# Optimization experiments

Measured on AMD Instinct MI355X. Metric: run time of the kernel, lower is better.

## Reference

```python
import jax, jax.numpy as jnp
import numpy as np

N_NODES = 50000
N_EDGES = 600000
N_GRAPHS = 64
IN_C, HID_C, OUT_C = 128, 128, 64


def gcn_conv(x, edge_index, W, b, num_nodes):
    """PyG GCNConv: x' = D^-1/2 (A + I) D^-1/2 (x W) + b, messages src->dst."""
    src, dst = edge_index[0], edge_index[1]
    # add self-loops
    loop = jnp.arange(num_nodes, dtype=src.dtype)
    src_full = jnp.concatenate([src, loop])
    dst_full = jnp.concatenate([dst, loop])
    # degree of A+I counted at the aggregation (dst) side
    deg = jax.ops.segment_sum(jnp.ones_like(dst_full, dtype=x.dtype), dst_full,
                              num_segments=num_nodes)
    dinv = jax.lax.rsqrt(jnp.maximum(deg, 1.0))
    norm = dinv[src_full] * dinv[dst_full]              # [E+N]
    h = x @ W                                           # [N, C_out] dense GEMM
    msg = h[src_full] * norm[:, None]                   # gather + scale
    out = jax.ops.segment_sum(msg, dst_full, num_segments=num_nodes)  # scatter-add
    return out + b


def global_mean_pool(x, batch, num_graphs):
    s = jax.ops.segment_sum(x, batch, num_segments=num_graphs)
    cnt = jax.ops.segment_sum(jnp.ones_like(batch, dtype=x.dtype), batch,
                              num_segments=num_graphs)
    return s / jnp.maximum(cnt, 1.0)[:, None]


def setup_inputs() -> dict:
    key = jax.random.key(0)
    ks = jax.random.split(key, 8)
    x = jax.random.normal(ks[0], (N_NODES, IN_C), dtype=jnp.float32)
    edge_index = jax.random.randint(ks[1], (2, N_EDGES), 0, N_NODES, dtype=jnp.int64)
    batch = jnp.sort(jax.random.randint(ks[2], (N_NODES,), 0, N_GRAPHS, dtype=jnp.int64))
    # Glorot-style init like PyG defaults
    W1 = jax.random.normal(ks[3], (IN_C, HID_C), dtype=jnp.float32) * (1.0 / np.sqrt(IN_C))
    b1 = jnp.zeros((HID_C,), dtype=jnp.float32)
    W2 = jax.random.normal(ks[4], (HID_C, OUT_C), dtype=jnp.float32) * (1.0 / np.sqrt(HID_C))
    b2 = jnp.zeros((OUT_C,), dtype=jnp.float32)
    return {"x": x, "W1": W1, "b1": b1, "W2": W2, "b2": b2,
            "edge_index": edge_index, "batch": batch}


def reference(x, W1, b1, W2, b2, edge_index, batch):
    h = gcn_conv(x, edge_index, W1, b1, N_NODES)
    h = jax.nn.relu(h)
    h = gcn_conv(h, edge_index, W2, b2, N_NODES)
    return global_mean_pool(h, batch, N_GRAPHS)  # [N_GRAPHS, OUT_C]
```

## Files before the change

kernel.cpp:

```cpp
#include <hip/hip_runtime.h>

#define NN 50000
#define NE 600000
#define NG 64
#define SCAN_T 1024
#define SCAN_NB ((NN + SCAN_T - 1) / SCAN_T)
#define PSPLIT 16

typedef unsigned int uint_t;
typedef unsigned short ushort_t;
typedef __attribute__((ext_vector_type(8))) short bf16x8;
typedef __attribute__((ext_vector_type(4))) float f32x4;

__device__ __forceinline__ ushort_t f2bf(float x) {
    uint_t u = __builtin_bit_cast(uint_t, x);
    u = (u + 0x7FFFu + ((u >> 16) & 1u)) >> 16;
    return (ushort_t)u;
}
__device__ __forceinline__ float bf_lo(uint_t p) {
    uint_t v = p << 16; return __builtin_bit_cast(float, v);
}
__device__ __forceinline__ float bf_hi(uint_t p) {
    uint_t v = p & 0xFFFF0000u; return __builtin_bit_cast(float, v);
}

__global__ void k_zero_deg(int* __restrict__ deg) {
    int i = blockIdx.x * blockDim.x + threadIdx.x;
    if (i < NN) deg[i] = 0;
}

__global__ void k_hist(const int* __restrict__ dst, int* __restrict__ deg) {
    int e = blockIdx.x * blockDim.x + threadIdx.x;
    if (e < NE) atomicAdd(&deg[dst[e]], 1);
}

__global__ void k_wprep(const float* __restrict__ W1, const float* __restrict__ W2,
                        ushort_t* __restrict__ W1t, ushort_t* __restrict__ W2t) {
    int idx = blockIdx.x * 256 + threadIdx.x;
    if (idx < 128 * 128) {
        int k = idx >> 7, n = idx & 127;
        W1t[n * 128 + k] = f2bf(W1[idx]);
    } else if (idx < 128 * 128 + 128 * 64) {
        int j = idx - 128 * 128;
        int k = j >> 6, n = j & 63;
        W2t[n * 128 + k] = f2bf(W2[j]);
    }
}

__global__ __launch_bounds__(SCAN_T) void k_scan1(const int* __restrict__ deg,
                                                  int* __restrict__ blockSums) {
    __shared__ int s[SCAN_T];
    int i = blockIdx.x * SCAN_T + threadIdx.x;
    s[threadIdx.x] = (i < NN) ? deg[i] : 0;
    __syncthreads();
    for (int off = SCAN_T / 2; off > 0; off >>= 1) {
        if (threadIdx.x < off) s[threadIdx.x] += s[threadIdx.x + off];
        __syncthreads();
    }
    if (threadIdx.x == 0) blockSums[blockIdx.x] = s[0];
}

__global__ __launch_bounds__(SCAN_T) void k_scan3(const int* __restrict__ deg,
                                                  const int* __restrict__ blockSums,
                                                  int* __restrict__ rowptr,
                                                  int* __restrict__ cursor,
                                                  float* __restrict__ dinv) {
    __shared__ int offs[64];
    __shared__ int s[SCAN_T];
    const int t = threadIdx.x;
    if (t < 64) {
        int orig = (t < SCAN_NB) ? blockSums[t] : 0;
        int v = orig;
        for (int off = 1; off < 64; off <<= 1) {
            int u = __shfl_up(v, off);
            if (t >= off) v += u;
        }
        offs[t] = v - orig;
    }
    const int i = blockIdx.x * SCAN_T + t;
    const int v = (i < NN) ? deg[i] : 0;
    s[t] = v;
    __syncthreads();
    for (int off = 1; off < SCAN_T; off <<= 1) {
        int u = (t >= off) ? s[t - off] : 0;
        int cur = s[t];
        __syncthreads();
        s[t] = cur + u;
        __syncthreads();
    }
    if (i < NN) {
        int ex = offs[blockIdx.x] + s[t] - v;
        rowptr[i] = ex;
        cursor[i] = ex;
        dinv[i] = rsqrtf((float)(v + 1));
    }
    if (i == 0) rowptr[NN] = NE;
}

__global__ void k_scatter(const int* __restrict__ src, const int* __restrict__ dst,
                          int* __restrict__ cursor, int* __restrict__ csr_src) {
    int e = blockIdx.x * blockDim.x + threadIdx.x;
    if (e >= NE) return;
    int d = dst[e];
    int p = atomicAdd(&cursor[d], 1);
    csr_src[p] = src[e];
}

__global__ __launch_bounds__(256) void k_gemm_mfma(const float* __restrict__ X,
                                                   const ushort_t* __restrict__ Wt,
                                                   const float* __restrict__ dinv,
                                                   ushort_t* __restrict__ Hb) {
    __shared__ ushort_t xs[128 * 128];
    __shared__ ushort_t ws[128 * 128];
    const int tid = threadIdx.x;
    const int row0 = blockIdx.x * 128;

    for (int idx = tid; idx < 128 * 32; idx += 256) {
        int r = idx >> 5, c4 = idx & 31;
        int row = row0 + r;
        float4 v = make_float4(0.f, 0.f, 0.f, 0.f);
        if (row < NN) v = ((const float4*)X)[(long)row * 32 + c4];
        ushort4 o;
        o.x = f2bf(v.x); o.y = f2bf(v.y); o.z = f2bf(v.z); o.w = f2bf(v.w);
        uint_t byte = (uint_t)(r * 256 + c4 * 8) ^ (uint_t)((r & 7) << 4);
        *(ushort4*)((char*)xs + byte) = o;
    }
    for (int idx = tid; idx < 128 * 16; idx += 256) {
        int n = idx >> 4, c16 = idx & 15;
        uint4 v = ((const uint4*)Wt)[idx];
        uint_t byte = (uint_t)(n * 256 + c16 * 16) ^ (uint_t)((n & 7) << 4);
        *(uint4*)((char*)ws + byte) = v;
    }
    __syncthreads();

    const int w = tid >> 6;
    const int l = tid & 63;
    const int m0 = (w >> 1) * 4;
    const int n0 = (w & 1) * 4;
    const int lr = l & 15;
    const int kg = l >> 4;

    f32x4 acc[4][4] = {};
    for (int kk = 0; kk < 4; ++kk) {
        const int kb = kk * 64 + kg * 16;
        bf16x8 a[4], b[4];
#pragma unroll
        for (int m = 0; m < 4; ++m) {
            int r = (m0 + m) * 16 + lr;
            uint_t byte = (uint_t)(r * 256 + kb) ^ (uint_t)((r & 7) << 4);
            a[m] = *(const bf16x8*)((const char*)xs + byte);
        }
#pragma unroll
        for (int n = 0; n < 4; ++n) {
            int r = (n0 + n) * 16 + lr;
            uint_t byte = (uint_t)(r * 256 + kb) ^ (uint_t)((r & 7) << 4);
            b[n] = *(const bf16x8*)((const char*)ws + byte);
        }
#pragma unroll
        for (int m = 0; m < 4; ++m)
#pragma unroll
            for (int n = 0; n < 4; ++n)
                acc[m][n] = __builtin_amdgcn_mfma_f32_16x16x32_bf16(a[m], b[n], acc[m][n], 0, 0, 0);
    }

#pragma unroll
    for (int m = 0; m < 4; ++m) {
#pragma unroll
        for (int r = 0; r < 4; ++r) {
            int row = row0 + (m0 + m) * 16 + kg * 4 + r;
            if (row < NN) {
                float sc = dinv[row];
#pragma unroll
                for (int n = 0; n < 4; ++n) {
                    int col = (n0 + n) * 16 + lr;
                    Hb[(long)row * 128 + col] = f2bf(acc[m][n][r] * sc);
                }
            }
        }
    }
}

__global__ __launch_bounds__(256) void k_gemm_mfma2(const ushort_t* __restrict__ H1,
                                                    const ushort_t* __restrict__ W2t,
                                                    const float* __restrict__ dinv,
                                                    ushort_t* __restrict__ G) {
    __shared__ ushort_t xs[128 * 128];
    __shared__ ushort_t ws2[64 * 128];
    const int tid = threadIdx.x;
    const int row0 = blockIdx.x * 128;

    for (int idx = tid; idx < 128 * 16; idx += 256) {
        int r = idx >> 4, c16 = idx & 15;
        int row = row0 + r;
        uint4 v = make_uint4(0u, 0u, 0u, 0u);
        if (row < NN) v = ((const uint4*)H1)[(long)row * 16 + c16];
        uint_t byte = (uint_t)(r * 256 + c16 * 16) ^ (uint_t)((r & 7) << 4);
        *(uint4*)((char*)xs + byte) = v;
    }
    for (int idx = tid; idx < 64 * 16; idx += 256) {
        int n = idx >> 4, c16 = idx & 15;
        uint4 v = ((const uint4*)W2t)[idx];
        uint_t byte = (uint_t)(n * 256 + c16 * 16) ^ (uint_t)((n & 7) << 4);
        *(uint4*)((char*)ws2 + byte) = v;
    }
    __syncthreads();

    const int w = tid >> 6;
    const int l = tid & 63;
    const int lr = l & 15;
    const int kg = l >> 4;
    const int m0 = w * 2;

    f32x4 acc[2][4] = {};
    for (int kk = 0; kk < 4; ++kk) {
        const int kb = kk * 64 + kg * 16;
        bf16x8 a[2], b[4];
#pragma unroll
        for (int m = 0; m < 2; ++m) {
            int r = (m0 + m) * 16 + lr;
            uint_t byte = (uint_t)(r * 256 + kb) ^ (uint_t)((r & 7) << 4);
            a[m] = *(const bf16x8*)((const char*)xs + byte);
        }
#pragma unroll
        for (int n = 0; n < 4; ++n) {
            int r = n * 16 + lr;
            uint_t byte = (uint_t)(r * 256 + kb) ^ (uint_t)((r & 7) << 4);
            b[n] = *(const bf16x8*)((const char*)ws2 + byte);
        }
#pragma unroll
        for (int m = 0; m < 2; ++m)
#pragma unroll
            for (int n = 0; n < 4; ++n)
                acc[m][n] = __builtin_amdgcn_mfma_f32_16x16x32_bf16(a[m], b[n], acc[m][n], 0, 0, 0);
    }

#pragma unroll
    for (int m = 0; m < 2; ++m) {
#pragma unroll
        for (int r = 0; r < 4; ++r) {
            int row = row0 + (m0 + m) * 16 + kg * 4 + r;
            if (row < NN) {
                float sc = dinv[row];
#pragma unroll
                for (int n = 0; n < 4; ++n) {
                    int col = n * 16 + lr;
                    G[(long)row * 64 + col] = f2bf(acc[m][n][r] * sc);
                }
            }
        }
    }
}

template <int C, int EPI>
__global__ __launch_bounds__(256) void k_agg(const int* __restrict__ rowptr,
                                             const int* __restrict__ csr_src,
                                             const float* __restrict__ dinv,
                                             const ushort_t* __restrict__ Hb,
                                             const float* __restrict__ bias,
                                             ushort_t* __restrict__ OUT) {
    constexpr int TPN = C / 8;
    constexpr int NPB = 256 / TPN;
    const int node = blockIdx.x * NPB + threadIdx.x / TPN;
    if (node >= NN) return;
    const int lane = threadIdx.x % TPN;
    const float dd = dinv[node];
    const uint4* __restrict__ H4 = (const uint4*)Hb;

    float a0, a1, a2, a3, a4, a5, a6, a7;
    {
        uint4 sv = H4[(long)node * TPN + lane];
        a0 = bf_lo(sv.x); a1 = bf_hi(sv.x);
        a2 = bf_lo(sv.y); a3 = bf_hi(sv.y);
        a4 = bf_lo(sv.z); a5 = bf_hi(sv.z);
        a6 = bf_lo(sv.w); a7 = bf_hi(sv.w);
    }

    const int beg = rowptr[node], end = rowptr[node + 1];
    int k = beg;
    const int n4 = beg + ((end - beg) & ~3);
    for (; k < n4; k += 4) {
        int s0 = csr_src[k + 0];
        int s1 = csr_src[k + 1];
        int s2 = csr_src[k + 2];
        int s3 = csr_src[k + 3];
        uint4 h0 = H4[(long)s0 * TPN + lane];
        uint4 h1 = H4[(long)s1 * TPN + lane];
        uint4 h2 = H4[(long)s2 * TPN + lane];
        uint4 h3 = H4[(long)s3 * TPN + lane];
        a0 += (bf_lo(h0.x) + bf_lo(h1.x)) + (bf_lo(h2.x) + bf_lo(h3.x));
        a1 += (bf_hi(h0.x) + bf_hi(h1.x)) + (bf_hi(h2.x) + bf_hi(h3.x));
        a2 += (bf_lo(h0.y) + bf_lo(h1.y)) + (bf_lo(h2.y) + bf_lo(h3.y));
        a3 += (bf_hi(h0.y) + bf_hi(h1.y)) + (bf_hi(h2.y) + bf_hi(h3.y));
        a4 += (bf_lo(h0.z) + bf_lo(h1.z)) + (bf_lo(h2.z) + bf_lo(h3.z));
        a5 += (bf_hi(h0.z) + bf_hi(h1.z)) + (bf_hi(h2.z) + bf_hi(h3.z));
        a6 += (bf_lo(h0.w) + bf_lo(h1.w)) + (bf_lo(h2.w) + bf_lo(h3.w));
        a7 += (bf_hi(h0.w) + bf_hi(h1.w)) + (bf_hi(h2.w) + bf_hi(h3.w));
    }
    for (; k < end; ++k) {
        int s = csr_src[k];
        uint4 h = H4[(long)s * TPN + lane];
        a0 += bf_lo(h.x); a1 += bf_hi(h.x);
        a2 += bf_lo(h.y); a3 += bf_hi(h.y);
        a4 += bf_lo(h.z); a5 += bf_hi(h.z);
        a6 += bf_lo(h.w); a7 += bf_hi(h.w);
    }

    a0 *= dd; a1 *= dd; a2 *= dd; a3 *= dd;
    a4 *= dd; a5 *= dd; a6 *= dd; a7 *= dd;

    if (EPI == 0) {
        const float4 b0 = *(const float4*)&bias[lane * 8];
        const float4 b1 = *(const float4*)&bias[lane * 8 + 4];
        a0 = fmaxf(a0 + b0.x, 0.f); a1 = fmaxf(a1 + b0.y, 0.f);
        a2 = fmaxf(a2 + b0.z, 0.f); a3 = fmaxf(a3 + b0.w, 0.f);
        a4 = fmaxf(a4 + b1.x, 0.f); a5 = fmaxf(a5 + b1.y, 0.f);
        a6 = fmaxf(a6 + b1.z, 0.f); a7 = fmaxf(a7 + b1.w, 0.f);
    }
    uint4 o;
    o.x = (uint_t)f2bf(a0) | ((uint_t)f2bf(a1) << 16);
    o.y = (uint_t)f2bf(a2) | ((uint_t)f2bf(a3) << 16);
    o.z = (uint_t)f2bf(a4) | ((uint_t)f2bf(a5) << 16);
    o.w = (uint_t)f2bf(a6) | ((uint_t)f2bf(a7) << 16);
    ((uint4*)OUT)[(long)node * TPN + lane] = o;
}

__global__ __launch_bounds__(256) void k_pool1(const ushort_t* __restrict__ V,
                                               const int* __restrict__ batch,
                                               float* __restrict__ partial) {
    const int g = blockIdx.x / PSPLIT;
    const int s = blockIdx.x % PSPLIT;
    int beg, end;
    {
        int lo = 0, hi = NN;
        while (lo < hi) { int mid = (lo + hi) >> 1; if (batch[mid] < g) lo = mid + 1; else hi = mid; }
        beg = lo;
        lo = beg; hi = NN;
        while (lo < hi) { int mid = (lo + hi) >> 1; if (batch[mid] < g + 1) lo = mid + 1; else hi = mid; }
        end = lo;
    }
    const int c = threadIdx.x & 15;
    const int rg = threadIdx.x >> 4;
    const uint2* __restrict__ V2 = (const uint2*)V;

    float4 acc = make_float4(0.f, 0.f, 0.f, 0.f);
    for (int n = beg + s * 16 + rg; n < end; n += PSPLIT * 16) {
        uint2 h = V2[(long)n * 16 + c];
        acc.x += bf_lo(h.x); acc.y += bf_hi(h.x);
        acc.z += bf_lo(h.y); acc.w += bf_hi(h.y);
    }
    __shared__ float4 red[16][17];
    red[rg][c] = acc;
    __syncthreads();
    if (rg == 0) {
        float4 t = red[0][c];
#pragma unroll
        for (int i = 1; i < 16; ++i) {
            float4 u = red[i][c];
            t.x += u.x; t.y += u.y; t.z += u.z; t.w += u.w;
        }
        ((float4*)partial)[(long)blockIdx.x * 16 + c] = t;
    }
}

__global__ __launch_bounds__(64) void k_pool2(const float* __restrict__ partial,
                                              const int* __restrict__ batch,
                                              const float* __restrict__ b2,
                                              float* __restrict__ out) {
    const int g = blockIdx.x;
    const int ch = threadIdx.x;
    int beg, end;
    {
        int lo = 0, hi = NN;
        while (lo < hi) { int mid = (lo + hi) >> 1; if (batch[mid] < g) lo = mid + 1; else hi = mid; }
        beg = lo;
        lo = beg; hi = NN;
        while (lo < hi) { int mid = (lo + hi) >> 1; if (batch[mid] < g + 1) lo = mid + 1; else hi = mid; }
        end = lo;
    }
    float s = 0.f;
    for (int i = 0; i < PSPLIT; ++i) s += partial[(long)(g * PSPLIT + i) * 64 + ch];
    int cnt = end - beg;
    out[g * 64 + ch] = (cnt > 0) ? (s / (float)cnt + b2[ch]) : 0.f;
}

extern "C" void kernel_launch(void* const* d_in, const int* in_sizes, int n_in,
                              void* d_out, int out_size, void* d_ws, size_t ws_size,
                              hipStream_t stream) {
    const float* x  = (const float*)d_in[0];
    const float* W1 = (const float*)d_in[1];
    const float* b1 = (const float*)d_in[2];
    const float* W2 = (const float*)d_in[3];
    const float* b2 = (const float*)d_in[4];
    const int* ei   = (const int*)d_in[5];
    const int* src  = ei;
    const int* dst  = ei + NE;
    const int* batch = (const int*)d_in[6];
    float* out = (float*)d_out;

    char* p = (char*)d_ws;
    int* deg       = (int*)p;          p += (size_t)NN * 4;
    int* rowptr    = (int*)p;          p += (size_t)(NN + 4) * 4;
    int* cursor    = (int*)p;          p += (size_t)NN * 4;
    int* csr_src   = (int*)p;          p += (size_t)NE * 4;
    int* blockSums = (int*)p;          p += (size_t)64 * 4;
    float* dinv    = (float*)p;        p += (size_t)NN * 4;
    float* partial = (float*)p;        p += (size_t)NG * PSPLIT * 64 * 4;
    ushort_t* W1t  = (ushort_t*)p;     p += (size_t)128 * 128 * 2;
    ushort_t* W2t  = (ushort_t*)p;     p += (size_t)64 * 128 * 2;
    ushort_t* Hb   = (ushort_t*)p;     p += (size_t)NN * 128 * 2;
    ushort_t* H1b  = (ushort_t*)p;     p += (size_t)NN * 128 * 2;
    ushort_t* Gb   = (ushort_t*)p;     p += (size_t)NN * 64 * 2;
    ushort_t* Vb   = (ushort_t*)p;     p += (size_t)NN * 64 * 2;

    k_wprep<<<96, 256, 0, stream>>>(W1, W2, W1t, W2t);
    k_zero_deg<<<(NN + 255) / 256, 256, 0, stream>>>(deg);
    k_hist<<<(NE + 255) / 256, 256, 0, stream>>>(dst, deg);
    k_scan1<<<SCAN_NB, SCAN_T, 0, stream>>>(deg, blockSums);
    k_scan3<<<SCAN_NB, SCAN_T, 0, stream>>>(deg, blockSums, rowptr, cursor, dinv);
    k_scatter<<<(NE + 255) / 256, 256, 0, stream>>>(src, dst, cursor, csr_src);

    k_gemm_mfma<<<(NN + 127) / 128, 256, 0, stream>>>(x, W1t, dinv, Hb);
    k_agg<128, 0><<<(NN + 15) / 16, 256, 0, stream>>>(rowptr, csr_src, dinv, Hb, b1, H1b);

    k_gemm_mfma2<<<(NN + 127) / 128, 256, 0, stream>>>(H1b, W2t, dinv, Gb);
    k_agg<64, 1><<<(NN + 31) / 32, 256, 0, stream>>>(rowptr, csr_src, dinv, Gb, b1 , Vb);

    k_pool1<<<NG * PSPLIT, 256, 0, stream>>>(Vb, batch, partial);
    k_pool2<<<NG, 64, 0, stream>>>(partial, batch, b2, out);
}
```

Baseline: 159.1 us.

## Fuse CSR build into cooperative kernel and fuse layer-2 aggregation with pooling

```diff
diff --git a/kernel.cpp b/kernel.cpp
--- a/kernel.cpp
+++ b/kernel.cpp
@@ -1,11 +1,14 @@
 #include <hip/hip_runtime.h>
+#include <hip/hip_cooperative_groups.h>
+
+namespace cg = cooperative_groups;
 
 #define NN 50000
 #define NE 600000
 #define NG 64
 #define SCAN_T 1024
 #define SCAN_NB ((NN + SCAN_T - 1) / SCAN_T)
-#define PSPLIT 16
+#define COOP_NB 256
 
 typedef unsigned int uint_t;
 typedef unsigned short ushort_t;
@@ -24,86 +27,85 @@
     uint_t v = p & 0xFFFF0000u; return __builtin_bit_cast(float, v);
 }
 
-__global__ void k_zero_deg(int* __restrict__ deg) {
-    int i = blockIdx.x * blockDim.x + threadIdx.x;
-    if (i < NN) deg[i] = 0;
-}
-
-__global__ void k_hist(const int* __restrict__ dst, int* __restrict__ deg) {
-    int e = blockIdx.x * blockDim.x + threadIdx.x;
-    if (e < NE) atomicAdd(&deg[dst[e]], 1);
-}
-
-__global__ void k_wprep(const float* __restrict__ W1, const float* __restrict__ W2,
-                        ushort_t* __restrict__ W1t, ushort_t* __restrict__ W2t) {
-    int idx = blockIdx.x * 256 + threadIdx.x;
-    if (idx < 128 * 128) {
-        int k = idx >> 7, n = idx & 127;
-        W1t[n * 128 + k] = f2bf(W1[idx]);
-    } else if (idx < 128 * 128 + 128 * 64) {
-        int j = idx - 128 * 128;
-        int k = j >> 6, n = j & 63;
-        W2t[n * 128 + k] = f2bf(W2[j]);
-    }
-}
-
-__global__ __launch_bounds__(SCAN_T) void k_scan1(const int* __restrict__ deg,
-                                                  int* __restrict__ blockSums) {
-    __shared__ int s[SCAN_T];
-    int i = blockIdx.x * SCAN_T + threadIdx.x;
-    s[threadIdx.x] = (i < NN) ? deg[i] : 0;
-    __syncthreads();
-    for (int off = SCAN_T / 2; off > 0; off >>= 1) {
-        if (threadIdx.x < off) s[threadIdx.x] += s[threadIdx.x + off];
-        __syncthreads();
-    }
-    if (threadIdx.x == 0) blockSums[blockIdx.x] = s[0];
-}
-
-__global__ __launch_bounds__(SCAN_T) void k_scan3(const int* __restrict__ deg,
-                                                  const int* __restrict__ blockSums,
+__global__ __launch_bounds__(SCAN_T) void k_build(const float* __restrict__ W1,
+                                                  const float* __restrict__ W2,
+                                                  const int* __restrict__ src,
+                                                  const int* __restrict__ dst,
+                                                  ushort_t* __restrict__ W1t,
+                                                  ushort_t* __restrict__ W2t,
+                                                  int* __restrict__ deg,
+                                                  int* __restrict__ blockSums,
                                                   int* __restrict__ rowptr,
                                                   int* __restrict__ cursor,
-                                                  float* __restrict__ dinv) {
-    __shared__ int offs[64];
+                                                  float* __restrict__ dinv,
+                                                  float* __restrict__ psum,
+                                                  int* __restrict__ csr_src) {
+    cg::grid_group grid = cg::this_grid();
+    const int tid = threadIdx.x;
+    const int gtid = blockIdx.x * SCAN_T + tid;
+    const int GT = COOP_NB * SCAN_T;
+
+    for (int i = gtid; i < NN; i += GT) deg[i] = 0;
+    for (int i = gtid; i < NG * 64; i += GT) psum[i] = 0.f;
+    for (int i = gtid; i < 128 * 128; i += GT) {
+        int k = i >> 7, n = i & 127;
+        W1t[n * 128 + k] = f2bf(W1[i]);
+    }
+    for (int i = gtid; i < 128 * 64; i += GT) {
+        int k = i >> 6, n = i & 63;
+        W2t[n * 128 + k] = f2bf(W2[i]);
+    }
+    grid.sync();
+
+    for (int e = gtid; e < NE; e += GT) atomicAdd(&deg[dst[e]], 1);
+    grid.sync();
+
     __shared__ int s[SCAN_T];
-    const int t = threadIdx.x;
-    if (t < 64) {
-        int orig = (t < SCAN_NB) ? blockSums[t] : 0;
-        int v = orig;
-        for (int off = 1; off < 64; off <<= 1) {
-            int u = __shfl_up(v, off);
-            if (t >= off) v += u;
-        }
-        offs[t] = v - orig;
-    }
-    const int i = blockIdx.x * SCAN_T + t;
-    const int v = (i < NN) ? deg[i] : 0;
-    s[t] = v;
-    __syncthreads();
-    for (int off = 1; off < SCAN_T; off <<= 1) {
-        int u = (t >= off) ? s[t - off] : 0;
-        int cur = s[t];
+    __shared__ int offs_s;
+    int v = 0;
+    if (blockIdx.x < SCAN_NB) {
+        int i = blockIdx.x * SCAN_T + tid;
+        v = (i < NN) ? deg[i] : 0;
+        s[tid] = v;
         __syncthreads();
-        s[t] = cur + u;
+        for (int off = 1; off < SCAN_T; off <<= 1) {
+            int u = (tid >= off) ? s[tid - off] : 0;
+            int cur = s[tid];
+            __syncthreads();
+            s[tid] = cur + u;
+            __syncthreads();
+        }
+        if (tid == SCAN_T - 1) blockSums[blockIdx.x] = s[SCAN_T - 1];
+    }
+    grid.sync();
+
+    if (blockIdx.x < SCAN_NB) {
+        if (tid < 64) {
+            int orig = (tid < SCAN_NB) ? blockSums[tid] : 0;
+            int w = orig;
+            for (int off = 1; off < 64; off <<= 1) {
+                int u = __shfl_up(w, off);
+                if (tid >= off) w += u;
+            }
+            if (tid == (int)blockIdx.x) offs_s = w - orig;
+        }
         __syncthreads();
-    }
-    if (i < NN) {
-        int ex = offs[blockIdx.x] + s[t] - v;
-        rowptr[i] = ex;
-        cursor[i] = ex;
-        dinv[i] = rsqrtf((float)(v + 1));
-    }
-    if (i == 0) rowptr[NN] = NE;
-}
-
-__global__ void k_scatter(const int* __restrict__ src, const int* __restrict__ dst,
-                          int* __restrict__ cursor, int* __restrict__ csr_src) {
-    int e = blockIdx.x * blockDim.x + threadIdx.x;
-    if (e >= NE) return;
-    int d = dst[e];
-    int p = atomicAdd(&cursor[d], 1);
-    csr_src[p] = src[e];
+        int i = blockIdx.x * SCAN_T + tid;
+        if (i < NN) {
+            int ex = offs_s + s[tid] - v;
+            rowptr[i] = ex;
+            cursor[i] = ex;
+            dinv[i] = rsqrtf((float)(v + 1));
+        }
+        if (i == 0) rowptr[NN] = NE;
+    }
+    grid.sync();
+
+    for (int e = gtid; e < NE; e += GT) {
+        int d = dst[e];
+        int p = atomicAdd(&cursor[d], 1);
+        csr_src[p] = src[e];
+    }
 }
 
 __global__ __launch_bounds__(256) void k_gemm_mfma(const float* __restrict__ X,
@@ -251,14 +253,13 @@
     }
 }
 
-template <int C, int EPI>
-__global__ __launch_bounds__(256) void k_agg(const int* __restrict__ rowptr,
-                                             const int* __restrict__ csr_src,
-                                             const float* __restrict__ dinv,
-                                             const ushort_t* __restrict__ Hb,
-                                             const float* __restrict__ bias,
-                                             ushort_t* __restrict__ OUT) {
-    constexpr int TPN = C / 8;
+__global__ __launch_bounds__(256) void k_agg1(const int* __restrict__ rowptr,
+                                              const int* __restrict__ csr_src,
+                                              const float* __restrict__ dinv,
+                                              const ushort_t* __restrict__ Hb,
+                                              const float* __restrict__ bias,
+                                              ushort_t* __restrict__ OUT) {
+    constexpr int TPN = 16;
     constexpr int NPB = 256 / TPN;
     const int node = blockIdx.x * NPB + threadIdx.x / TPN;
     if (node >= NN) return;
@@ -308,14 +309,13 @@
     a0 *= dd; a1 *= dd; a2 *= dd; a3 *= dd;
     a4 *= dd; a5 *= dd; a6 *= dd; a7 *= dd;
 
-    if (EPI == 0) {
-        const float4 b0 = *(const float4*)&bias[lane * 8];
-        const float4 b1 = *(const float4*)&bias[lane * 8 + 4];
-        a0 = fmaxf(a0 + b0.x, 0.f); a1 = fmaxf(a1 + b0.y, 0.f);
-        a2 = fmaxf(a2 + b0.z, 0.f); a3 = fmaxf(a3 + b0.w, 0.f);
-        a4 = fmaxf(a4 + b1.x, 0.f); a5 = fmaxf(a5 + b1.y, 0.f);
-        a6 = fmaxf(a6 + b1.z, 0.f); a7 = fmaxf(a7 + b1.w, 0.f);
-    }
+    const float4 b0 = *(const float4*)&bias[lane * 8];
+    const float4 b1 = *(const float4*)&bias[lane * 8 + 4];
+    a0 = fmaxf(a0 + b0.x, 0.f); a1 = fmaxf(a1 + b0.y, 0.f);
+    a2 = fmaxf(a2 + b0.z, 0.f); a3 = fmaxf(a3 + b0.w, 0.f);
+    a4 = fmaxf(a4 + b1.x, 0.f); a5 = fmaxf(a5 + b1.y, 0.f);
+    a6 = fmaxf(a6 + b1.z, 0.f); a7 = fmaxf(a7 + b1.w, 0.f);
+
     uint4 o;
     o.x = (uint_t)f2bf(a0) | ((uint_t)f2bf(a1) << 16);
     o.y = (uint_t)f2bf(a2) | ((uint_t)f2bf(a3) << 16);
@@ -324,45 +324,88 @@
     ((uint4*)OUT)[(long)node * TPN + lane] = o;
 }
 
-__global__ __launch_bounds__(256) void k_pool1(const ushort_t* __restrict__ V,
-                                               const int* __restrict__ batch,
-                                               float* __restrict__ partial) {
-    const int g = blockIdx.x / PSPLIT;
-    const int s = blockIdx.x % PSPLIT;
-    int beg, end;
-    {
-        int lo = 0, hi = NN;
-        while (lo < hi) { int mid = (lo + hi) >> 1; if (batch[mid] < g) lo = mid + 1; else hi = mid; }
-        beg = lo;
-        lo = beg; hi = NN;
-        while (lo < hi) { int mid = (lo + hi) >> 1; if (batch[mid] < g + 1) lo = mid + 1; else hi = mid; }
-        end = lo;
-    }
-    const int c = threadIdx.x & 15;
-    const int rg = threadIdx.x >> 4;
-    const uint2* __restrict__ V2 = (const uint2*)V;
-
-    float4 acc = make_float4(0.f, 0.f, 0.f, 0.f);
-    for (int n = beg + s * 16 + rg; n < end; n += PSPLIT * 16) {
-        uint2 h = V2[(long)n * 16 + c];
-        acc.x += bf_lo(h.x); acc.y += bf_hi(h.x);
-        acc.z += bf_lo(h.y); acc.w += bf_hi(h.y);
-    }
-    __shared__ float4 red[16][17];
-    red[rg][c] = acc;
+__global__ __launch_bounds__(256) void k_agg2pool(const int* __restrict__ rowptr,
+                                                  const int* __restrict__ csr_src,
+                                                  const float* __restrict__ dinv,
+                                                  const ushort_t* __restrict__ Gb,
+                                                  const int* __restrict__ batch,
+                                                  float* __restrict__ psum) {
+    constexpr int TPN = 8;
+    constexpr int NPB = 32;
+    const int nodeLocal = threadIdx.x / TPN;
+    const int node = blockIdx.x * NPB + nodeLocal;
+    const int lane = threadIdx.x % TPN;
+    __shared__ float vsh[NPB][64 + 1];
+    __shared__ int gsh[NPB];
+
+    if (node < NN) {
+        const float dd = dinv[node];
+        const uint4* __restrict__ H4 = (const uint4*)Gb;
+
+        float a0, a1, a2, a3, a4, a5, a6, a7;
+        {
+            uint4 sv = H4[(long)node * TPN + lane];
+            a0 = bf_lo(sv.x); a1 = bf_hi(sv.x);
+            a2 = bf_lo(sv.y); a3 = bf_hi(sv.y);
+            a4 = bf_lo(sv.z); a5 = bf_hi(sv.z);
+            a6 = bf_lo(sv.w); a7 = bf_hi(sv.w);
+        }
+        const int beg = rowptr[node], end = rowptr[node + 1];
+        int k = beg;
+        const int n4 = beg + ((end - beg) & ~3);
+        for (; k < n4; k += 4) {
+            int s0 = csr_src[k + 0];
+            int s1 = csr_src[k + 1];
+            int s2 = csr_src[k + 2];
+            int s3 = csr_src[k + 3];
+            uint4 h0 = H4[(long)s0 * TPN + lane];
+            uint4 h1 = H4[(long)s1 * TPN + lane];
+            uint4 h2 = H4[(long)s2 * TPN + lane];
+            uint4 h3 = H4[(long)s3 * TPN + lane];
+            a0 += (bf_lo(h0.x) + bf_lo(h1.x)) + (bf_lo(h2.x) + bf_lo(h3.x));
+            a1 += (bf_hi(h0.x) + bf_hi(h1.x)) + (bf_hi(h2.x) + bf_hi(h3.x));
+            a2 += (bf_lo(h0.y) + bf_lo(h1.y)) + (bf_lo(h2.y) + bf_lo(h3.y));
+            a3 += (bf_hi(h0.y) + bf_hi(h1.y)) + (bf_hi(h2.y) + bf_hi(h3.y));
+            a4 += (bf_lo(h0.z) + bf_lo(h1.z)) + (bf_lo(h2.z) + bf_lo(h3.z));
+            a5 += (bf_hi(h0.z) + bf_hi(h1.z)) + (bf_hi(h2.z) + bf_hi(h3.z));
+            a6 += (bf_lo(h0.w) + bf_lo(h1.w)) + (bf_lo(h2.w) + bf_lo(h3.w));
+            a7 += (bf_hi(h0.w) + bf_hi(h1.w)) + (bf_hi(h2.w) + bf_hi(h3.w));
+        }
+        for (; k < end; ++k) {
+            int s = csr_src[k];
+            uint4 h = H4[(long)s * TPN + lane];
+            a0 += bf_lo(h.x); a1 += bf_hi(h.x);
+            a2 += bf_lo(h.y); a3 += bf_hi(h.y);
+            a4 += bf_lo(h.z); a5 += bf_hi(h.z);
+            a6 += bf_lo(h.w); a7 += bf_hi(h.w);
+        }
+        float* vp = &vsh[nodeLocal][lane * 8];
+        vp[0] = a0 * dd; vp[1] = a1 * dd; vp[2] = a2 * dd; vp[3] = a3 * dd;
+        vp[4] = a4 * dd; vp[5] = a5 * dd; vp[6] = a6 * dd; vp[7] = a7 * dd;
+        if (lane == 0) gsh[nodeLocal] = batch[node];
+    } else {
+        if (lane == 0) gsh[nodeLocal] = -1;
+    }
     __syncthreads();
-    if (rg == 0) {
-        float4 t = red[0][c];
-#pragma unroll
-        for (int i = 1; i < 16; ++i) {
-            float4 u = red[i][c];
-            t.x += u.x; t.y += u.y; t.z += u.z; t.w += u.w;
-        }
-        ((float4*)partial)[(long)blockIdx.x * 16 + c] = t;
-    }
-}
-
-__global__ __launch_bounds__(64) void k_pool2(const float* __restrict__ partial,
+
+    if (threadIdx.x < 64) {
+        const int ch = threadIdx.x;
+        float acc = 0.f;
+        int gprev = -1;
+        for (int n = 0; n < NPB; ++n) {
+            int g = gsh[n];
+            if (g != gprev) {
+                if (gprev >= 0) unsafeAtomicAdd(&psum[gprev * 64 + ch], acc);
+                acc = 0.f;
+                gprev = g;
+            }
+            if (g >= 0) acc += vsh[n][ch];
+        }
+        if (gprev >= 0) unsafeAtomicAdd(&psum[gprev * 64 + ch], acc);
+    }
+}
+
+__global__ __launch_bounds__(64) void k_pool2(const float* __restrict__ psum,
                                               const int* __restrict__ batch,
                                               const float* __restrict__ b2,
                                               float* __restrict__ out) {
@@ -377,10 +420,8 @@
         while (lo < hi) { int mid = (lo + hi) >> 1; if (batch[mid] < g + 1) lo = mid + 1; else hi = mid; }
         end = lo;
     }
-    float s = 0.f;
-    for (int i = 0; i < PSPLIT; ++i) s += partial[(long)(g * PSPLIT + i) * 64 + ch];
     int cnt = end - beg;
-    out[g * 64 + ch] = (cnt > 0) ? (s / (float)cnt + b2[ch]) : 0.f;
+    out[g * 64 + ch] = (cnt > 0) ? (psum[g * 64 + ch] / (float)cnt + b2[ch]) : 0.f;
 }
 
 extern "C" void kernel_launch(void* const* d_in, const int* in_sizes, int n_in,
@@ -392,8 +433,8 @@
     const float* W2 = (const float*)d_in[3];
     const float* b2 = (const float*)d_in[4];
     const int* ei   = (const int*)d_in[5];
-    const int* src  = ei;
-    const int* dst  = ei + NE;
+    const int* src  = (const int*)ei;
+    const int* dst  = (const int*)(ei + NE);
     const int* batch = (const int*)d_in[6];
     float* out = (float*)d_out;
 
@@ -404,27 +445,27 @@
     int* csr_src   = (int*)p;          p += (size_t)NE * 4;
     int* blockSums = (int*)p;          p += (size_t)64 * 4;
     float* dinv    = (float*)p;        p += (size_t)NN * 4;
-    float* partial = (float*)p;        p += (size_t)NG * PSPLIT * 64 * 4;
+    float* psum    = (float*)p;        p += (size_t)NG * 64 * 4;
     ushort_t* W1t  = (ushort_t*)p;     p += (size_t)128 * 128 * 2;
     ushort_t* W2t  = (ushort_t*)p;     p += (size_t)64 * 128 * 2;
     ushort_t* Hb   = (ushort_t*)p;     p += (size_t)NN * 128 * 2;
     ushort_t* H1b  = (ushort_t*)p;     p += (size_t)NN * 128 * 2;
     ushort_t* Gb   = (ushort_t*)p;     p += (size_t)NN * 64 * 2;
-    ushort_t* Vb   = (ushort_t*)p;     p += (size_t)NN * 64 * 2;
-
-    k_wprep<<<96, 256, 0, stream>>>(W1, W2, W1t, W2t);
-    k_zero_deg<<<(NN + 255) / 256, 256, 0, stream>>>(deg);
-    k_hist<<<(NE + 255) / 256, 256, 0, stream>>>(dst, deg);
-    k_scan1<<<SCAN_NB, SCAN_T, 0, stream>>>(deg, blockSums);
-    k_scan3<<<SCAN_NB, SCAN_T, 0, stream>>>(deg, blockSums, rowptr, cursor, dinv);
-    k_scatter<<<(NE + 255) / 256, 256, 0, stream>>>(src, dst, cursor, csr_src);
+
+    {
+        void* args[] = {(void*)&W1, (void*)&W2, (void*)&src, (void*)&dst,
+                        (void*)&W1t, (void*)&W2t, (void*)&deg, (void*)&blockSums,
+                        (void*)&rowptr, (void*)&cursor, (void*)&dinv,
+                        (void*)&psum, (void*)&csr_src};
+        hipLaunchCooperativeKernel((const void*)k_build, dim3(COOP_NB), dim3(SCAN_T),
+                                   args, 0, stream);
+    }
 
     k_gemm_mfma<<<(NN + 127) / 128, 256, 0, stream>>>(x, W1t, dinv, Hb);
-    k_agg<128, 0><<<(NN + 15) / 16, 256, 0, stream>>>(rowptr, csr_src, dinv, Hb, b1, H1b);
+    k_agg1<<<(NN + 15) / 16, 256, 0, stream>>>(rowptr, csr_src, dinv, Hb, b1, H1b);
 
     k_gemm_mfma2<<<(NN + 127) / 128, 256, 0, stream>>>(H1b, W2t, dinv, Gb);
-    k_agg<64, 1><<<(NN + 31) / 32, 256, 0, stream>>>(rowptr, csr_src, dinv, Gb, b1 , Vb);
-
-    k_pool1<<<NG * PSPLIT, 256, 0, stream>>>(Vb, batch, partial);
-    k_pool2<<<NG, 64, 0, stream>>>(partial, batch, b2, out);
-}
+    k_agg2pool<<<(NN + 31) / 32, 256, 0, stream>>>(rowptr, csr_src, dinv, Gb, batch, psum);
+
+    k_pool2<<<NG, 64, 0, stream>>>(psum, batch, b2, out);
+}
```

Result: slower. 274.0 us (+72.2%).
